# Optimization experiments

Hardware: AMD Instinct MI355X
Metric: run time of the kernel (lower is better)

## Reference

```python
import jax, jax.numpy as jnp
import numpy as np

V, E, H, H2, T, B, S = 50000, 300, 512, 256, 10, 64, 256
START_IDX, STOP_IDX = 8, 9


def setup_inputs() -> dict:
    key = jax.random.key(0)
    ks = jax.random.split(key, 16)
    sd = 1.0 / np.sqrt(H2)
    inp = {
        'sentence': jax.random.randint(ks[0], (B, S), 0, V, dtype=jnp.int32),
        'emb': jax.random.normal(ks[1], (V, E), jnp.float32),
        'wih_f': jax.random.uniform(ks[2], (4 * H2, E), jnp.float32, -sd, sd),
        'whh_f': jax.random.uniform(ks[3], (4 * H2, H2), jnp.float32, -sd, sd),
        'bih_f': jax.random.uniform(ks[4], (4 * H2,), jnp.float32, -sd, sd),
        'bhh_f': jax.random.uniform(ks[5], (4 * H2,), jnp.float32, -sd, sd),
        'wih_b': jax.random.uniform(ks[6], (4 * H2, E), jnp.float32, -sd, sd),
        'whh_b': jax.random.uniform(ks[7], (4 * H2, H2), jnp.float32, -sd, sd),
        'bih_b': jax.random.uniform(ks[8], (4 * H2,), jnp.float32, -sd, sd),
        'bhh_b': jax.random.uniform(ks[9], (4 * H2,), jnp.float32, -sd, sd),
        'W_out': jax.random.uniform(ks[10], (T, H), jnp.float32, -1.0 / np.sqrt(H), 1.0 / np.sqrt(H)),
        'b_out': jax.random.uniform(ks[11], (T,), jnp.float32, -1.0 / np.sqrt(H), 1.0 / np.sqrt(H)),
        'h0': jax.random.normal(ks[12], (2, B, H2), jnp.float32),
        'c0': jax.random.normal(ks[13], (2, B, H2), jnp.float32),
    }
    trans = jax.random.normal(ks[14], (T, T), jnp.float32)
    trans = trans.at[START_IDX, :].set(-10000.0).at[:, STOP_IDX].set(-10000.0)
    inp['transitions'] = trans
    return inp


def _lstm_dir(x, h0, c0, wih, whh, bih, bhh, reverse):
    # x: (S, B, E); returns hidden states (S, B, H2)
    def step(carry, xt):
        h, c = carry
        g = xt @ wih.T + bih + h @ whh.T + bhh  # (B, 4*H2)
        i, f, gg, o = jnp.split(g, 4, axis=-1)  # PyTorch gate order i,f,g,o
        c = jax.nn.sigmoid(f) * c + jax.nn.sigmoid(i) * jnp.tanh(gg)
        h = jax.nn.sigmoid(o) * jnp.tanh(c)
        return (h, c), h
    _, hs = jax.lax.scan(step, (h0, c0), x, reverse=reverse)
    return hs


def _features(sentence, emb, wih_f, whh_f, bih_f, bhh_f, wih_b, whh_b, bih_b, bhh_b,
              W_out, b_out, h0, c0):
    # Replicate torch's .view(seq,batch,-1): raw memory reinterpretation of (B,S,E)
    embeds = emb[sentence].reshape(S, B, E)
    h_f = _lstm_dir(embeds, h0[0], c0[0], wih_f, whh_f, bih_f, bhh_f, False)
    h_b = _lstm_dir(embeds, h0[1], c0[1], wih_b, whh_b, bih_b, bhh_b, True)
    lstm_out = jnp.concatenate([h_f, h_b], axis=-1)  # (S, B, H)
    # Replicate torch's .view(batch,-1,hidden): reinterpretation, not transpose
    lstm_out = lstm_out.reshape(B, S, H)
    return lstm_out @ W_out.T + b_out  # (B, S, T)


def _viterbi(feats, transitions):
    # feats: (B, S, T)
    init = jnp.full((B, T), -10000.0, feats.dtype).at[:, START_IDX].set(0.0)

    def step(fv, feat_t):
        # ntv[b, next, prev] = fv[b, prev] + transitions[next, prev]
        ntv = fv[:, None, :] + transitions[None, :, :]
        vv = jnp.max(ntv, axis=2)          # (B, T)
        bp = jnp.argmax(ntv, axis=2)       # (B, T) backpointers
        return vv + feat_t, bp

    fv, bps = jax.lax.scan(step, init, jnp.swapaxes(feats, 0, 1))  # bps: (S, B, T)
    terminal = fv + transitions[STOP_IDX]
    path_score = jnp.max(terminal, axis=1)[:, None]   # (B, 1)
    last_tag = jnp.argmax(terminal, axis=1)           # (B,)

    def back(best, bp):
        return bp[jnp.arange(B), best], best

    _, path = jax.lax.scan(back, last_tag, bps, reverse=True)  # (S, B)
    return path_score, path.T  # (B, 1), (B, S)


def reference(sentence, emb, wih_f, whh_f, bih_f, bhh_f, wih_b, whh_b, bih_b, bhh_b,
              W_out, b_out, transitions, h0, c0):
    feats = _features(sentence, emb, wih_f, whh_f, bih_f, bhh_f,
                      wih_b, whh_b, bih_b, bhh_b, W_out, b_out, h0, c0)
    return _viterbi(feats, transitions)
```

## Files before the change

kernel.cpp:

```cpp
#include <hip/hip_runtime.h>
#include <hip/hip_cooperative_groups.h>

namespace cg = cooperative_groups;

#define E_    300
#define H2_   256
#define T_    10
#define B_    64
#define S_    256
#define G_    (S_*B_)
#define GATES (4*H2_)
#define KVR   192
#define KLD   64
#define WPITCH4 17

__global__ void prep_kernel(const float* __restrict__ whh_f, const float* __restrict__ whh_b,
                            const float* __restrict__ bih_f, const float* __restrict__ bhh_f,
                            const float* __restrict__ bih_b, const float* __restrict__ bhh_b,
                            float* __restrict__ wpack, float* __restrict__ bsum) {
    int idx = blockIdx.x * blockDim.x + threadIdx.x;
    if (idx < 2 * 2 * H2_ * 512) {
        int dhf = idx >> 17;
        int d = dhf >> 1, hf = dhf & 1;
        int rem = idx & 131071;
        int k = rem >> 9;
        int t = rem & 511;
        int r = ((t >> 7) << 8) + hf * 128 + (t & 127);
        const float* w = d ? whh_b : whh_f;
        wpack[idx] = w[r * H2_ + k];
    }
    if (idx < 2 * GATES) {
        int d = idx >> 10, j = idx & 1023;
        bsum[idx] = d ? (bih_b[j] + bhh_b[j]) : (bih_f[j] + bhh_f[j]);
    }
}

__global__ __launch_bounds__(256) void xproj_kernel(
    const int* __restrict__ sent, const float* __restrict__ emb,
    const float* __restrict__ wih_f, const float* __restrict__ wih_b,
    const float* __restrict__ bsum, float* __restrict__ xp) {
    __shared__ float As[128 * 21];
    __shared__ float Bs[20 * 64];
    __shared__ int   toks[128];
    int gt = blockIdx.x, jt = blockIdx.y, d = blockIdx.z;
    const float* wih = d ? wih_b : wih_f;
    int tid = threadIdx.x;
    int g0 = gt * 128, j0 = jt * 64;
    if (tid < 128) toks[tid] = sent[g0 + tid];
    __syncthreads();

    int ty = tid >> 4, tx = tid & 15;
    float acc[8][4];
    float4 bv = *(const float4*)&bsum[d * 1024 + j0 + tx * 4];
    #pragma unroll
    for (int i = 0; i < 8; i++) { acc[i][0] = bv.x; acc[i][1] = bv.y; acc[i][2] = bv.z; acc[i][3] = bv.w; }

    for (int kt = 0; kt < 15; kt++) {
        int k0 = kt * 20;
        #pragma unroll
        for (int l = 0; l < 10; l++) {
            int e = l * 256 + tid; int i = e / 20, k = e % 20;
            As[i * 21 + k] = emb[(long)toks[i] * E_ + k0 + k];
        }
        #pragma unroll
        for (int l = 0; l < 5; l++) {
            int e = l * 256 + tid; int k = e >> 6, j = e & 63;
            Bs[k * 64 + j] = wih[(j0 + j) * E_ + k0 + k];
        }
        __syncthreads();
        #pragma unroll
        for (int k = 0; k < 20; k++) {
            float4 b4 = *(const float4*)&Bs[k * 64 + tx * 4];
            #pragma unroll
            for (int i = 0; i < 8; i++) {
                float a = As[(ty * 8 + i) * 21 + k];
                acc[i][0] += a * b4.x; acc[i][1] += a * b4.y;
                acc[i][2] += a * b4.z; acc[i][3] += a * b4.w;
            }
        }
        __syncthreads();
    }
    #pragma unroll
    for (int i = 0; i < 8; i++) {
        float4 o; o.x = acc[i][0]; o.y = acc[i][1]; o.z = acc[i][2]; o.w = acc[i][3];
        *(float4*)&xp[((long)d * G_ + g0 + ty * 8 + i) * 1024 + j0 + tx * 4] = o;
    }
}

__global__ __launch_bounds__(512, 2) void lstm_kernel(
    const float* __restrict__ xp, const float* __restrict__ wpack,
    const float* __restrict__ h0, const float* __restrict__ c0,
    float* __restrict__ hcat, unsigned long long* __restrict__ mbox) {
    __shared__ float  h_lds[256];
    __shared__ float  g_lds[512];
    __shared__ float4 wlds[512 * WPITCH4];

    int t = threadIdx.x;
    int blk = blockIdx.x;
    int p = blk >> 1, hf = blk & 1;
    int d = p >> 6, b = p & 63;
    const float* wp = wpack + (long)((d * 2 + hf) * 256) * 512;

    float wreg[KVR];
    #pragma unroll
    for (int k = 0; k < KVR; k++) {
        wreg[k] = wp[(long)k * 512 + t];
        asm volatile("" : "+v"(wreg[k]));
    }
    #pragma unroll
    for (int k = KVR; k < 256; k += 4) {
        float4 wv;
        wv.x = wp[(long)(k + 0) * 512 + t];
        wv.y = wp[(long)(k + 1) * 512 + t];
        wv.z = wp[(long)(k + 2) * 512 + t];
        wv.w = wp[(long)(k + 3) * 512 + t];
        wlds[t * WPITCH4 + ((k - KVR) >> 2)] = wv;
    }
    cg::this_grid().sync();

    float c = 0.f;
    if (t < 256) h_lds[t] = h0[(d * B_ + b) * H2_ + t];
    if (t < 128) c = c0[(d * B_ + b) * H2_ + hf * 128 + t];
    __syncthreads();

    unsigned long long* mb_out = mbox + (size_t)((p * 2 + hf) * 2) * 128;
    unsigned long long* mb_in  = mbox + (size_t)((p * 2 + (1 - hf)) * 2) * 128;
    const long xbase = (long)d * G_ * 1024;
    const int  r = ((t >> 7) << 8) + hf * 128 + (t & 127);

    for (int step = 0; step < S_; step++) {
        int s = d ? (S_ - 1 - step) : step;
        int g = s * B_ + b;
        float acc = xp[xbase + (long)g * 1024 + r];
        const float4* h4 = (const float4*)h_lds;
        #pragma unroll
        for (int j = 0; j < KVR / 4; j++) {
            float4 hv = h4[j];
            acc += wreg[4*j+0] * hv.x + wreg[4*j+1] * hv.y
                 + wreg[4*j+2] * hv.z + wreg[4*j+3] * hv.w;
        }
        #pragma unroll
        for (int j = 0; j < KLD / 4; j++) {
            float4 wv = wlds[t * WPITCH4 + j];
            float4 hv = h4[KVR / 4 + j];
            acc += wv.x * hv.x + wv.y * hv.y + wv.z * hv.z + wv.w * hv.w;
        }
        g_lds[t] = acc;
        __syncthreads();
        if (t < 128) {
            float iv = g_lds[t],        fv = g_lds[128 + t];
            float gv = g_lds[256 + t],  ov = g_lds[384 + t];
            float si = 1.f / (1.f + __expf(-iv));
            float sf = 1.f / (1.f + __expf(-fv));
            float so = 1.f / (1.f + __expf(-ov));
            float tg = tanhf(gv);
            c = sf * c + si * tg;
            float h = so * tanhf(c);
            h_lds[hf * 128 + t] = h;
            union { float f; unsigned u; } cv; cv.f = h;
            __hip_atomic_store(&mb_out[(step & 1) * 128 + t],
                               ((unsigned long long)(unsigned)(step + 1) << 32) | cv.u,
                               __ATOMIC_RELAXED, __HIP_MEMORY_SCOPE_AGENT);
            hcat[(long)g * 512 + d * 256 + hf * 128 + t] = h;
        } else if (t < 256) {
            int u = t - 128;
            unsigned want = (unsigned)(step + 1);
            unsigned long long w;
            do {
                w = __hip_atomic_load(&mb_in[(step & 1) * 128 + u],
                                      __ATOMIC_RELAXED, __HIP_MEMORY_SCOPE_AGENT);
            } while ((unsigned)(w >> 32) != want);
            union { unsigned u32; float f; } cv; cv.u32 = (unsigned)w;
            h_lds[(1 - hf) * 128 + u] = cv.f;
        }
        __syncthreads();
    }
}

__global__ void feats_kernel(const float* __restrict__ hcat, const float* __restrict__ Wout,
                             const float* __restrict__ bout, float* __restrict__ feats) {
    int tid = threadIdx.x; int w = tid >> 6, l = tid & 63;
    int g = blockIdx.x * 4 + w;
    float r[8];
    #pragma unroll
    for (int m = 0; m < 8; m++) r[m] = hcat[(long)g * 512 + m * 64 + l];
    #pragma unroll
    for (int tt = 0; tt < 10; tt++) {
        float a = 0.f;
        #pragma unroll
        for (int m = 0; m < 8; m++) a += r[m] * Wout[tt * 512 + m * 64 + l];
        #pragma unroll
        for (int off = 32; off > 0; off >>= 1) a += __shfl_down(a, off);
        if (l == 0) feats[g * 10 + tt] = a + bout[tt];
    }
}

__global__ void viterbi_kernel(const float* __restrict__ feats, const float* __restrict__ trans,
                               float* __restrict__ out) {
    __shared__ unsigned char bp[256 * 16];
    int l = threadIdx.x; int b = blockIdx.x;
    float trrow[10];
    #pragma unroll
    for (int p = 0; p < 10; p++) trrow[p] = (l < 10) ? trans[l * 10 + p] : 0.f;
    float tr_stop = (l < 10) ? trans[90 + l] : -3e38f;
    float fv = (l == 8) ? 0.f : -10000.f;

    for (int s = 0; s < 256; s++) {
        float m = -3e38f; int arg = 0;
        #pragma unroll
        for (int p = 0; p < 10; p++) {
            float v = __shfl(fv, p) + trrow[p];
            if (v > m) { m = v; arg = p; }
        }
        float ft = (l < 10) ? feats[((long)b * 256 + s) * 10 + l] : 0.f;
        fv = m + ft;
        if (l < 10) bp[s * 16 + l] = (unsigned char)arg;
    }
    __syncthreads();
    float term = fv + tr_stop;
    float best = -3e38f; int bt = 0;
    #pragma unroll
    for (int p = 0; p < 10; p++) {
        float v = __shfl(term, p);
        if (v > best) { best = v; bt = p; }
    }
    if (l == 0) {
        out[b] = best;
        int cur = bt;
        out[64 + b * 256 + 255] = (float)cur;
        for (int s = 254; s >= 0; s--) {
            cur = bp[(s + 1) * 16 + cur];
            out[64 + b * 256 + s] = (float)cur;
        }
    }
}

extern "C" void kernel_launch(void* const* d_in, const int* in_sizes, int n_in,
                              void* d_out, int out_size, void* d_ws, size_t ws_size,
                              hipStream_t stream) {
    const int*   sent  = (const int*)  d_in[0];
    const float* emb   = (const float*)d_in[1];
    const float* wih_f = (const float*)d_in[2];
    const float* whh_f = (const float*)d_in[3];
    const float* bih_f = (const float*)d_in[4];
    const float* bhh_f = (const float*)d_in[5];
    const float* wih_b = (const float*)d_in[6];
    const float* whh_b = (const float*)d_in[7];
    const float* bih_b = (const float*)d_in[8];
    const float* bhh_b = (const float*)d_in[9];
    const float* Wout  = (const float*)d_in[10];
    const float* bout  = (const float*)d_in[11];
    const float* h0    = (const float*)d_in[12];
    const float* c0    = (const float*)d_in[13];
    const float* trans = (const float*)d_in[14];

    float* ws    = (float*)d_ws;
    float* xp    = ws;
    float* hcat  = ws + 33554432;
    float* wpack = ws + 41943040;
    float* bsum  = ws + 42467328;
    float* feats = ws;
    unsigned long long* mbox = (unsigned long long*)(ws + 41943040);
    float* out   = (float*)d_out;

    hipLaunchKernelGGL(prep_kernel, dim3(2048), dim3(256), 0, stream,
                       whh_f, whh_b, bih_f, bhh_f, bih_b, bhh_b, wpack, bsum);
    hipLaunchKernelGGL(xproj_kernel, dim3(128, 16, 2), dim3(256), 0, stream,
                       sent, emb, wih_f, wih_b, bsum, xp);

    void* lstm_args[] = { (void*)&xp, (void*)&wpack, (void*)&h0, (void*)&c0,
                          (void*)&hcat, (void*)&mbox };
    hipLaunchCooperativeKernel((const void*)lstm_kernel, dim3(256), dim3(512),
                               lstm_args, 0, stream);

    hipLaunchKernelGGL(feats_kernel, dim3(4096), dim3(256), 0, stream,
                       hcat, Wout, bout, feats);
    hipLaunchKernelGGL(viterbi_kernel, dim3(64), dim3(64), 0, stream,
                       feats, trans, out);
}
```

Measured before the change: 1.519 ms.

## Split LSTM recurrence across 8 hidden-unit slices sharing 4 batch rows per block

Each block now handles 4 batch rows and one of 8 hidden-unit slices. A slice's weights live in 64 registers per thread plus LDS, and are reused across the 4 batch elements. Each step, a block gathers the other 7 slices' h values through mailbox polling instead of a single partner block. The mailbox moves to its own workspace region, which lets the grid-wide sync after weight loading be dropped. The next step's input projection is also prefetched. This cuts register pressure and weight-reuse cost, but adds more cross-block synchronisation per step and likely non-broadcast LDS reads of h.

```diff
diff --git a/kernel.cpp b/kernel.cpp
--- a/kernel.cpp
+++ b/kernel.cpp
@@ -1,31 +1,26 @@
 #include <hip/hip_runtime.h>
-#include <hip/hip_cooperative_groups.h>
-
-namespace cg = cooperative_groups;
 
 #define E_    300
 #define H2_   256
-#define T_    10
 #define B_    64
 #define S_    256
 #define G_    (S_*B_)
 #define GATES (4*H2_)
-#define KVR   192
-#define KLD   64
-#define WPITCH4 17
+#define KREG  64
+#define WP4   49
+#define HP    260
 
 __global__ void prep_kernel(const float* __restrict__ whh_f, const float* __restrict__ whh_b,
                             const float* __restrict__ bih_f, const float* __restrict__ bhh_f,
                             const float* __restrict__ bih_b, const float* __restrict__ bhh_b,
                             float* __restrict__ wpack, float* __restrict__ bsum) {
     int idx = blockIdx.x * blockDim.x + threadIdx.x;
-    if (idx < 2 * 2 * H2_ * 512) {
-        int dhf = idx >> 17;
-        int d = dhf >> 1, hf = dhf & 1;
-        int rem = idx & 131071;
-        int k = rem >> 9;
-        int t = rem & 511;
-        int r = ((t >> 7) << 8) + hf * 128 + (t & 127);
+    if (idx < 2 * 8 * 128 * 256) {
+        int d  = idx >> 18;
+        int s  = (idx >> 15) & 7;
+        int rr = (idx >> 8) & 127;
+        int k  = idx & 255;
+        int r  = ((rr >> 5) << 8) + s * 32 + (rr & 31);
         const float* w = d ? whh_b : whh_f;
         wpack[idx] = w[r * H2_ + k];
     }
@@ -91,89 +86,108 @@
     const float* __restrict__ xp, const float* __restrict__ wpack,
     const float* __restrict__ h0, const float* __restrict__ c0,
     float* __restrict__ hcat, unsigned long long* __restrict__ mbox) {
-    __shared__ float  h_lds[256];
-    __shared__ float  g_lds[512];
-    __shared__ float4 wlds[512 * WPITCH4];
+    __shared__ float4 wlds[128 * WP4];
+    __shared__ float  h_lds[4 * HP];
+    __shared__ float  g_stage[512];
 
     int t = threadIdx.x;
-    int blk = blockIdx.x;
-    int p = blk >> 1, hf = blk & 1;
-    int d = p >> 6, b = p & 63;
-    const float* wp = wpack + (long)((d * 2 + hf) * 256) * 512;
-
-    float wreg[KVR];
-    #pragma unroll
-    for (int k = 0; k < KVR; k++) {
-        wreg[k] = wp[(long)k * 512 + t];
-        asm volatile("" : "+v"(wreg[k]));
-    }
-    #pragma unroll
-    for (int k = KVR; k < 256; k += 4) {
-        float4 wv;
-        wv.x = wp[(long)(k + 0) * 512 + t];
-        wv.y = wp[(long)(k + 1) * 512 + t];
-        wv.z = wp[(long)(k + 2) * 512 + t];
-        wv.w = wp[(long)(k + 3) * 512 + t];
-        wlds[t * WPITCH4 + ((k - KVR) >> 2)] = wv;
-    }
-    cg::this_grid().sync();
-
+    int bid = blockIdx.x;
+    int x = bid & 7, rest = bid >> 3;
+    int s = rest & 7, Ghi = rest >> 3;
+    int G = Ghi * 8 + x;
+    int d = G >> 4, bg = G & 15;
+    int j = t & 3, rr = t >> 2;
+    int q = rr >> 5, uu = rr & 31;
+    int r = q * 256 + s * 32 + uu;
+    int b = bg * 4 + j;
+
+    const float* wp = wpack + (size_t)((d * 8 + s) * 128) * 256;
+
+    float4 wr[16];
+    #pragma unroll
+    for (int kk = 0; kk < 16; kk++) wr[kk] = ((const float4*)(wp + rr * 256))[kk];
+
+    for (int e = t; e < 128 * 48; e += 512) {
+        int rrow = e / 48, kk = e % 48;
+        wlds[rrow * WP4 + kk] = ((const float4*)(wp + rrow * 256 + KREG))[kk];
+    }
+    for (int e = t; e < 1024; e += 512) {
+        int jj = e >> 8, u = e & 255;
+        h_lds[jj * HP + u] = h0[(d * B_ + bg * 4 + jj) * H2_ + u];
+    }
     float c = 0.f;
-    if (t < 256) h_lds[t] = h0[(d * B_ + b) * H2_ + t];
-    if (t < 128) c = c0[(d * B_ + b) * H2_ + hf * 128 + t];
+    if (t < 128) c = c0[(d * B_ + b) * H2_ + s * 32 + uu];
+
+    unsigned long long* mb_out = mbox + (size_t)(G * 8 + s) * 256;
+    const float* xq = xp + (size_t)d * G_ * 1024 + r;
+    float xcur;
+    {
+        int s0 = d ? 255 : 0;
+        xcur = xq[(size_t)(s0 * 64 + b) * 1024];
+    }
     __syncthreads();
 
-    unsigned long long* mb_out = mbox + (size_t)((p * 2 + hf) * 2) * 128;
-    unsigned long long* mb_in  = mbox + (size_t)((p * 2 + (1 - hf)) * 2) * 128;
-    const long xbase = (long)d * G_ * 1024;
-    const int  r = ((t >> 7) << 8) + hf * 128 + (t & 127);
-
     for (int step = 0; step < S_; step++) {
-        int s = d ? (S_ - 1 - step) : step;
-        int g = s * B_ + b;
-        float acc = xp[xbase + (long)g * 1024 + r];
-        const float4* h4 = (const float4*)h_lds;
-        #pragma unroll
-        for (int j = 0; j < KVR / 4; j++) {
-            float4 hv = h4[j];
-            acc += wreg[4*j+0] * hv.x + wreg[4*j+1] * hv.y
-                 + wreg[4*j+2] * hv.z + wreg[4*j+3] * hv.w;
-        }
-        #pragma unroll
-        for (int j = 0; j < KLD / 4; j++) {
-            float4 wv = wlds[t * WPITCH4 + j];
-            float4 hv = h4[KVR / 4 + j];
-            acc += wv.x * hv.x + wv.y * hv.y + wv.z * hv.z + wv.w * hv.w;
-        }
-        g_lds[t] = acc;
-        __syncthreads();
+        float xnext = 0.f;
+        int sn = d ? (254 - step) : (step + 1);
+        if (step < 255) xnext = xq[(size_t)(sn * 64 + b) * 1024];
+
+        const float4* hj = (const float4*)&h_lds[j * HP];
+        float a0 = xcur, a1 = 0.f, a2 = 0.f, a3 = 0.f;
+        #pragma unroll
+        for (int kk = 0; kk < 16; kk++) {
+            float4 hv = hj[kk];
+            a0 += wr[kk].x * hv.x; a1 += wr[kk].y * hv.y;
+            a2 += wr[kk].z * hv.z; a3 += wr[kk].w * hv.w;
+        }
+        const float4* wrow = &wlds[rr * WP4];
+        #pragma unroll
+        for (int kk = 0; kk < 48; kk++) {
+            float4 wv = wrow[kk]; float4 hv = hj[16 + kk];
+            a0 += wv.x * hv.x; a1 += wv.y * hv.y;
+            a2 += wv.z * hv.z; a3 += wv.w * hv.w;
+        }
+        g_stage[t] = (a0 + a1) + (a2 + a3);
+        __syncthreads();
+
+        int sidx = d ? (255 - step) : step;
         if (t < 128) {
-            float iv = g_lds[t],        fv = g_lds[128 + t];
-            float gv = g_lds[256 + t],  ov = g_lds[384 + t];
+            float iv = g_stage[t],        fv = g_stage[128 + t];
+            float gv = g_stage[256 + t],  ov = g_stage[384 + t];
             float si = 1.f / (1.f + __expf(-iv));
             float sf = 1.f / (1.f + __expf(-fv));
             float so = 1.f / (1.f + __expf(-ov));
             float tg = tanhf(gv);
             c = sf * c + si * tg;
             float h = so * tanhf(c);
-            h_lds[hf * 128 + t] = h;
+            h_lds[j * HP + s * 32 + uu] = h;
             union { float f; unsigned u; } cv; cv.f = h;
             __hip_atomic_store(&mb_out[(step & 1) * 128 + t],
                                ((unsigned long long)(unsigned)(step + 1) << 32) | cv.u,
                                __ATOMIC_RELAXED, __HIP_MEMORY_SCOPE_AGENT);
-            hcat[(long)g * 512 + d * 256 + hf * 128 + t] = h;
-        } else if (t < 256) {
-            int u = t - 128;
-            unsigned want = (unsigned)(step + 1);
-            unsigned long long w;
-            do {
-                w = __hip_atomic_load(&mb_in[(step & 1) * 128 + u],
-                                      __ATOMIC_RELAXED, __HIP_MEMORY_SCOPE_AGENT);
-            } while ((unsigned)(w >> 32) != want);
-            union { unsigned u32; float f; } cv; cv.u32 = (unsigned)w;
-            h_lds[(1 - hf) * 128 + u] = cv.f;
-        }
-        __syncthreads();
+            hcat[(size_t)(sidx * 64 + b) * 512 + d * 256 + s * 32 + uu] = h;
+        } else {
+            int v = t - 128;
+            #pragma unroll
+            for (int it = 0; it < 3; it++) {
+                int vv = v + it * 384;
+                if (vv < 896) {
+                    int spr = vv >> 7;
+                    int sp = spr + (spr >= s ? 1 : 0);
+                    int w = vv & 127;
+                    unsigned long long* ad =
+                        mbox + (size_t)(G * 8 + sp) * 256 + (step & 1) * 128 + w;
+                    unsigned long long val;
+                    do {
+                        val = __hip_atomic_load(ad, __ATOMIC_RELAXED, __HIP_MEMORY_SCOPE_AGENT);
+                    } while ((unsigned)(val >> 32) != (unsigned)(step + 1));
+                    union { unsigned u; float f; } cv; cv.u = (unsigned)val;
+                    h_lds[(w & 3) * HP + sp * 32 + (w >> 2)] = cv.f;
+                }
+            }
+        }
+        __syncthreads();
+        xcur = xnext;
     }
 }
 
@@ -259,8 +273,8 @@
     float* hcat  = ws + 33554432;
     float* wpack = ws + 41943040;
     float* bsum  = ws + 42467328;
+    unsigned long long* mbox = (unsigned long long*)(ws + 42469376);
     float* feats = ws;
-    unsigned long long* mbox = (unsigned long long*)(ws + 41943040);
     float* out   = (float*)d_out;
 
     hipLaunchKernelGGL(prep_kernel, dim3(2048), dim3(256), 0, stream,
```

Result: no change. 1.537 ms (+1.1%).
